# Optimization experiments

Hardware: AMD Instinct MI355X
Metric: run time of the kernel (lower is better)

Reference implementation:

```python
import jax, jax.numpy as jnp
import numpy as np

HIDDEN = 4096
HEAD_DIM = 128
N_HEADS = 32
N_KV_HEADS = 8
ROPE_THETA = 10000.0


def setup_inputs() -> dict:
    key = jax.random.key(0)
    k1, k2, k3 = jax.random.split(key, 3)
    qkv_dim = (N_HEADS + 2 * N_KV_HEADS) * HEAD_DIM  # 6144
    x = jax.random.normal(k1, (2, 2048, HIDDEN), dtype=jnp.float32)
    w_qkv = jax.random.normal(k2, (HIDDEN, qkv_dim), dtype=jnp.float32) * (HIDDEN ** -0.5)
    w_out = jax.random.normal(k3, (N_HEADS * HEAD_DIM, HIDDEN), dtype=jnp.float32) * ((N_HEADS * HEAD_DIM) ** -0.5)
    return {"x": x, "w_qkv": w_qkv, "w_out": w_out}


def _apply_rope(t):
    # t: [B, S, H, D], rotate over full head dim (half-split convention)
    B, S, H, D = t.shape
    half = D // 2
    inv_freq = 1.0 / (ROPE_THETA ** (jnp.arange(0, half, dtype=jnp.float32) / half))
    freqs = jnp.arange(S, dtype=jnp.float32)[:, None] * inv_freq[None, :]  # [S, D/2]
    cos = jnp.cos(freqs)[None, :, None, :].astype(t.dtype)
    sin = jnp.sin(freqs)[None, :, None, :].astype(t.dtype)
    t1, t2 = t[..., :half], t[..., half:]
    return jnp.concatenate([t1 * cos - t2 * sin, t1 * sin + t2 * cos], axis=-1)


def reference(x, w_qkv, w_out):
    B, S, _ = x.shape
    qkv = x @ w_qkv  # [B, S, (H + 2*Hkv) * D]
    qkv = qkv.reshape(B, S, N_HEADS + 2 * N_KV_HEADS, HEAD_DIM)
    q = qkv[:, :, :N_HEADS]                                 # [B,S,H,D]
    k = qkv[:, :, N_HEADS:N_HEADS + N_KV_HEADS]             # [B,S,Hkv,D]
    v = qkv[:, :, N_HEADS + N_KV_HEADS:]                    # [B,S,Hkv,D]
    q = _apply_rope(q)
    k = _apply_rope(k)
    # GQA: expand KV heads to match query heads
    group = N_HEADS // N_KV_HEADS
    k = jnp.repeat(k, group, axis=2)  # [B,S,H,D]
    v = jnp.repeat(v, group, axis=2)
    q = q.transpose(0, 2, 1, 3)  # [B,H,S,D]
    k = k.transpose(0, 2, 1, 3)
    v = v.transpose(0, 2, 1, 3)
    scale = HEAD_DIM ** -0.5
    scores = jnp.einsum('bhqd,bhkd->bhqk', q, k) * scale  # [B,H,S,S]
    probs = jax.nn.softmax(scores, axis=-1)
    out = jnp.einsum('bhqk,bhkd->bhqd', probs, v)  # [B,H,S,D]
    out = out.transpose(0, 2, 1, 3).reshape(B, S, N_HEADS * HEAD_DIM)
    return out @ w_out  # [B,S,hidden]
```

## Files before the change

### kernel.cpp

```cpp
#include <hip/hip_runtime.h>

typedef unsigned short u16;
typedef float f32x4 __attribute__((ext_vector_type(4)));
typedef __bf16 bf16x8 __attribute__((ext_vector_type(8)));

__device__ __forceinline__ u16 f2bf(float f) {
  union { float f; unsigned int u; } x; x.f = f;
  unsigned int u = x.u;
  u += 0x7fffu + ((u >> 16) & 1u);
  return (u16)(u >> 16);
}
__device__ __forceinline__ float bf2f(u16 h) {
  union { unsigned int u; float f; } x; x.u = ((unsigned int)h) << 16;
  return x.f;
}
#if __has_builtin(__builtin_amdgcn_exp2f)
__device__ __forceinline__ float exp2_hw(float x) { return __builtin_amdgcn_exp2f(x); }
#else
__device__ __forceinline__ float exp2_hw(float x) { return exp2f(x); }
#endif
__device__ __forceinline__ void load_lds16(const void* g, void* l) {
  __builtin_amdgcn_global_load_lds(
      (const __attribute__((address_space(1))) unsigned int*)g,
      (__attribute__((address_space(3))) unsigned int*)l, 16, 0, 0);
}
__device__ __forceinline__ f32x4 mfma16(bf16x8 a, bf16x8 b, f32x4 c) {
  return __builtin_amdgcn_mfma_f32_16x16x32_bf16(a, b, c, 0, 0, 0);
}
__device__ __forceinline__ void bar() { __builtin_amdgcn_s_barrier(); }
template <int Nw> __device__ __forceinline__ void waitvm() {
  if constexpr (Nw == 8)      asm volatile("s_waitcnt vmcnt(8)" ::: "memory");
  else if constexpr (Nw == 6) asm volatile("s_waitcnt vmcnt(6)" ::: "memory");
  else if constexpr (Nw == 4) asm volatile("s_waitcnt vmcnt(4)" ::: "memory");
  else                        asm volatile("s_waitcnt vmcnt(0)" ::: "memory");
}
__device__ __forceinline__ void phase_open() {
  asm volatile("" ::: "memory");
  __builtin_amdgcn_s_barrier();
  asm volatile("" ::: "memory");
  __builtin_amdgcn_s_setprio(1);
}
__device__ __forceinline__ void phase_close() {
  __builtin_amdgcn_s_setprio(0);
  asm volatile("" ::: "memory");
  __builtin_amdgcn_s_barrier();
  asm volatile("" ::: "memory");
}
template <int NV> __device__ __forceinline__ void phase_close_vm() {
  __builtin_amdgcn_s_setprio(0);
  asm volatile("" ::: "memory");
  waitvm<NV>();
  __builtin_amdgcn_s_barrier();
  asm volatile("" ::: "memory");
}

__global__ void convert4(const float* __restrict__ in, u16* __restrict__ out) {
  int i = blockIdx.x * blockDim.x + threadIdx.x;
  float4 v = reinterpret_cast<const float4*>(in)[i];
  ushort4 o;
  o.x = f2bf(v.x); o.y = f2bf(v.y); o.z = f2bf(v.z); o.w = f2bf(v.w);
  reinterpret_cast<ushort4*>(out)[i] = o;
}

__global__ void transpose_f32_bf16(const float* __restrict__ in, u16* __restrict__ out,
                                   int R, int Cd) {
  __shared__ float tile[32][33];
  int c0 = blockIdx.x * 32, r0 = blockIdx.y * 32;
  int tx = threadIdx.x, ty = threadIdx.y;
#pragma unroll
  for (int i = 0; i < 4; ++i)
    tile[ty + 8 * i][tx] = in[(size_t)(r0 + ty + 8 * i) * Cd + c0 + tx];
  __syncthreads();
#pragma unroll
  for (int i = 0; i < 4; ++i)
    out[(size_t)(c0 + ty + 8 * i) * R + r0 + tx] = f2bf(tile[tx][ty + 8 * i]);
}

__global__ void rope_table(float2* __restrict__ tab) {
  int i = blockIdx.x * blockDim.x + threadIdx.x;
  int s = i >> 6, d2 = i & 63;
  float inv = powf(10000.f, -(float)d2 * (1.f / 64.f));
  float fr = (float)s * inv;
  tab[i] = make_float2(cosf(fr), sinf(fr));
}

__global__ void rope_apply(u16* __restrict__ qkv, const float2* __restrict__ tab) {
  int i = blockIdx.x * blockDim.x + threadIdx.x;
  int d2 = i & 63;
  int head = (i >> 6) % 40;
  int row = i / 2560;
  size_t base = (size_t)row * 6144 + head * 128 + d2;
  float t1 = bf2f(qkv[base]), t2 = bf2f(qkv[base + 64]);
  float2 cs = tab[(row & 2047) * 64 + d2];
  float o1 = t1 * cs.x - t2 * cs.y;
  float o2 = t1 * cs.y + t2 * cs.x;
  float sc = (head < 32) ? 0.12751731654059898f : 1.f;
  qkv[base]      = f2bf(o1 * sc);
  qkv[base + 64] = f2bf(o2 * sc);
}

__global__ void build_vT(const u16* __restrict__ qkv, u16* __restrict__ vT) {
  __shared__ u16 tile[32][33];
  int st = blockIdx.x, dt = blockIdx.y, bh = blockIdx.z;
  int b = bh >> 3, hkv = bh & 7;
  int tx = threadIdx.x, ty = threadIdx.y;
  int s0 = st * 32, d0 = dt * 32;
#pragma unroll
  for (int i = 0; i < 4; ++i)
    tile[ty + 8 * i][tx] =
        qkv[(size_t)(b * 2048 + s0 + ty + 8 * i) * 6144 + 5120 + hkv * 128 + d0 + tx];
  __syncthreads();
  int s = s0 + tx;
  int sl = s & 63;
  int sp = (s & ~63) | (sl & 0x23) | ((sl & 0x0C) << 1) | ((sl & 0x10) >> 2);
#pragma unroll
  for (int i = 0; i < 4; ++i)
    vT[((size_t)bh * 128 + d0 + ty + 8 * i) * 2048 + sp] = tile[tx][ty + 8 * i];
}

template <int OUT_BF16>
__global__ __launch_bounds__(512, 2) void gemm_g1(const u16* __restrict__ A,
                                                  const u16* __restrict__ BT,
                                                  void* __restrict__ Cv,
                                                  int M, int N, int K) {
  __shared__ u16 As[3][256][64];
  __shared__ u16 Bs[3][128][64];
  const int tid = threadIdx.x, lane = tid & 63, wave = tid >> 6;
  const int lr = lane & 15, lg = lane >> 4, l7 = lane & 7;
  const int wm = wave >> 1, wn = wave & 1;
  const int nbx = N / 128;
  int bid = blockIdx.x;
  const int cpx = (int)gridDim.x >> 3;
  bid = (bid & 7) * cpx + (bid >> 3);
  const int bm = (bid / nbx) * 256, bn = (bid % nbx) * 128;
  const int NT = K / 64;
  const int ch0 = (lg ^ l7) << 3, ch1 = ((4 | lg) ^ l7) << 3;

  auto stageA = [&](int t, int rg) {
    int k0 = t * 64;
#pragma unroll
    for (int o = 0; o < 4; ++o) {
      int cid = o * 512 + tid;
      int row = cid >> 3;
      int sc2 = (cid & 7) ^ (row & 7);
      load_lds16(A + (size_t)(bm + row) * K + k0 + sc2 * 8,
                 (u16*)&As[rg][0][0] + (o * 512 + wave * 64) * 8);
    }
  };
  auto stageB = [&](int t, int rg) {
    int k0 = t * 64;
#pragma unroll
    for (int o = 0; o < 2; ++o) {
      int cid = o * 512 + tid;
      int row = cid >> 3;
      int sc2 = (cid & 7) ^ (row & 7);
      load_lds16(BT + (size_t)(bn + row) * K + k0 + sc2 * 8,
                 (u16*)&Bs[rg][0][0] + (o * 512 + wave * 64) * 8);
    }
  };

  bf16x8 af[4][2], b01[2][2], b23[2][2];
  f32x4 acc[4][4] = {};

  stageB(0, 0); stageA(0, 0); stageB(1, 1); stageA(1, 1);
  waitvm<6>();
  bar();

  int c = 0;
  for (int t = 0; t < NT; ++t) {
    int cs = c + 2; if (cs >= 3) cs -= 3;
    const bool pf = (t + 2) < NT;
#pragma unroll
    for (int mi = 0; mi < 4; ++mi) {
      af[mi][0] = *(const bf16x8*)&As[c][wm * 64 + mi * 16 + lr][ch0];
      af[mi][1] = *(const bf16x8*)&As[c][wm * 64 + mi * 16 + lr][ch1];
    }
#pragma unroll
    for (int j = 0; j < 2; ++j) {
      b01[j][0] = *(const bf16x8*)&Bs[c][wn * 64 + j * 16 + lr][ch0];
      b01[j][1] = *(const bf16x8*)&Bs[c][wn * 64 + j * 16 + lr][ch1];
    }
    if (pf) stageB(t + 2, cs);
    phase_open();
#pragma unroll
    for (int mi = 0; mi < 4; ++mi)
#pragma unroll
      for (int j = 0; j < 2; ++j) {
        acc[mi][j] = mfma16(af[mi][0], b01[j][0], acc[mi][j]);
        acc[mi][j] = mfma16(af[mi][1], b01[j][1], acc[mi][j]);
      }
    phase_close();
#pragma unroll
    for (int j = 0; j < 2; ++j) {
      b23[j][0] = *(const bf16x8*)&Bs[c][wn * 64 + (j + 2) * 16 + lr][ch0];
      b23[j][1] = *(const bf16x8*)&Bs[c][wn * 64 + (j + 2) * 16 + lr][ch1];
    }
    if (pf) stageA(t + 2, cs);
    phase_open();
#pragma unroll
    for (int mi = 0; mi < 4; ++mi)
#pragma unroll
      for (int j = 0; j < 2; ++j) {
        acc[mi][j + 2] = mfma16(af[mi][0], b23[j][0], acc[mi][j + 2]);
        acc[mi][j + 2] = mfma16(af[mi][1], b23[j][1], acc[mi][j + 2]);
      }
    if (pf) phase_close_vm<6>(); else phase_close_vm<0>();
    c = c + 1; if (c >= 3) c -= 3;
  }
#pragma unroll
  for (int mi = 0; mi < 4; ++mi) {
    int row = bm + wm * 64 + mi * 16 + lg * 4;
#pragma unroll
    for (int j = 0; j < 4; ++j) {
      int col = bn + wn * 64 + j * 16 + lr;
#pragma unroll
      for (int r = 0; r < 4; ++r) {
        if constexpr (OUT_BF16)
          ((u16*)Cv)[(size_t)(row + r) * N + col] = f2bf(acc[mi][j][r]);
        else
          ((float*)Cv)[(size_t)(row + r) * N + col] = acc[mi][j][r];
      }
    }
  }
}

template <int OUT_BF16>
__global__ __launch_bounds__(512, 2) void gemm_g2(const u16* __restrict__ A,
                                                  const u16* __restrict__ BT,
                                                  void* __restrict__ Cv,
                                                  int M, int N, int K) {
  __shared__ u16 As[2][256][64];
  __shared__ u16 Bs[2][256][64];
  const int tid = threadIdx.x, lane = tid & 63, wave = tid >> 6;
  const int lr = lane & 15, lg = lane >> 4, l7 = lane & 7;
  const int wm = wave >> 2, wn = wave & 3;
  const int nbx = N / 256;
  int bid = blockIdx.x;
  const int cpx = (int)gridDim.x >> 3;
  bid = (bid & 7) * cpx + (bid >> 3);
  const int bm = (bid / nbx) * 256, bn = (bid % nbx) * 256;
  const int NT = K / 64;
  const int ch0 = (lg ^ l7) << 3, ch1 = ((4 | lg) ^ l7) << 3;

  auto stageA = [&](int t, int rg) {
    int k0 = t * 64;
#pragma unroll
    for (int o = 0; o < 4; ++o) {
      int cid = o * 512 + tid;
      int row = cid >> 3;
      int sc2 = (cid & 7) ^ (row & 7);
      load_lds16(A + (size_t)(bm + row) * K + k0 + sc2 * 8,
                 (u16*)&As[rg][0][0] + (o * 512 + wave * 64) * 8);
    }
  };
  auto stageBh = [&](int t, int rg, int h) {
    int k0 = t * 64;
#pragma unroll
    for (int o = 0; o < 2; ++o) {
      int oo = h * 2 + o;
      int cid = oo * 512 + tid;
      int row = cid >> 3;
      int sc2 = (cid & 7) ^ (row & 7);
      load_lds16(BT + (size_t)(bn + row) * K + k0 + sc2 * 8,
                 (u16*)&Bs[rg][0][0] + (oo * 512 + wave * 64) * 8);
    }
  };

  bf16x8 a0[4][2], a1[4][2], b01[2][2], b23[2][2];
  f32x4 acc[8][4] = {};

  stageA(0, 0); stageBh(0, 0, 0); stageBh(0, 0, 1); stageA(1, 1);
  stageBh(1, 1, 0); stageBh(1, 1, 1);
  waitvm<8>();
  bar();

  for (int t = 0; t < NT; ++t) {
    const int c = t & 1;
    const bool pf = (t + 2) < NT;
#pragma unroll
    for (int mi = 0; mi < 4; ++mi) {
      a0[mi][0] = *(const bf16x8*)&As[c][wm * 128 + mi * 16 + lr][ch0];
      a0[mi][1] = *(const bf16x8*)&As[c][wm * 128 + mi * 16 + lr][ch1];
    }
#pragma unroll
    for (int j = 0; j < 2; ++j) {
      b01[j][0] = *(const bf16x8*)&Bs[c][wn * 64 + j * 16 + lr][ch0];
      b01[j][1] = *(const bf16x8*)&Bs[c][wn * 64 + j * 16 + lr][ch1];
    }
    phase_open();
#pragma unroll
    for (int mi = 0; mi < 4; ++mi)
#pragma unroll
      for (int j = 0; j < 2; ++j) {
        acc[mi][j] = mfma16(a0[mi][0], b01[j][0], acc[mi][j]);
        acc[mi][j] = mfma16(a0[mi][1], b01[j][1], acc[mi][j]);
      }
    phase_close();
#pragma unroll
    for (int j = 0; j < 2; ++j) {
      b23[j][0] = *(const bf16x8*)&Bs[c][wn * 64 + (j + 2) * 16 + lr][ch0];
      b23[j][1] = *(const bf16x8*)&Bs[c][wn * 64 + (j + 2) * 16 + lr][ch1];
    }
    phase_open();
#pragma unroll
    for (int mi = 0; mi < 4; ++mi)
#pragma unroll
      for (int j = 0; j < 2; ++j) {
        acc[mi][j + 2] = mfma16(a0[mi][0], b23[j][0], acc[mi][j + 2]);
        acc[mi][j + 2] = mfma16(a0[mi][1], b23[j][1], acc[mi][j + 2]);
      }
    phase_close();
#pragma unroll
    for (int mi = 0; mi < 4; ++mi) {
      a1[mi][0] = *(const bf16x8*)&As[c][wm * 128 + 64 + mi * 16 + lr][ch0];
      a1[mi][1] = *(const bf16x8*)&As[c][wm * 128 + 64 + mi * 16 + lr][ch1];
    }
    if (pf) stageBh(t + 2, c, 0);
    phase_open();
#pragma unroll
    for (int mi = 0; mi < 4; ++mi)
#pragma unroll
      for (int j = 0; j < 2; ++j) {
        acc[mi + 4][j] = mfma16(a1[mi][0], b01[j][0], acc[mi + 4][j]);
        acc[mi + 4][j] = mfma16(a1[mi][1], b01[j][1], acc[mi + 4][j]);
      }
    phase_close();
    if (pf) { stageBh(t + 2, c, 1); stageA(t + 2, c); }
    phase_open();
#pragma unroll
    for (int mi = 0; mi < 4; ++mi)
#pragma unroll
      for (int j = 0; j < 2; ++j) {
        acc[mi + 4][j + 2] = mfma16(a1[mi][0], b23[j][0], acc[mi + 4][j + 2]);
        acc[mi + 4][j + 2] = mfma16(a1[mi][1], b23[j][1], acc[mi + 4][j + 2]);
      }
    if (pf) phase_close_vm<8>(); else phase_close_vm<0>();
  }
#pragma unroll
  for (int mi = 0; mi < 8; ++mi) {
    int row = bm + wm * 128 + mi * 16 + lg * 4;
#pragma unroll
    for (int j = 0; j < 4; ++j) {
      int col = bn + wn * 64 + j * 16 + lr;
#pragma unroll
      for (int r = 0; r < 4; ++r) {
        if constexpr (OUT_BF16)
          ((u16*)Cv)[(size_t)(row + r) * N + col] = f2bf(acc[mi][j][r]);
        else
          ((float*)Cv)[(size_t)(row + r) * N + col] = acc[mi][j][r];
      }
    }
  }
}

__global__ __launch_bounds__(256, 3) void attn_fused(const u16* __restrict__ qkv,
                                                     const u16* __restrict__ vT,
                                                     u16* __restrict__ attn_out) {
  __shared__ u16 Ksm[64][128];
  __shared__ u16 Vsm[128][64];
  const int qt = blockIdx.x, h = blockIdx.y, b = blockIdx.z;
  const int hkv = h >> 2;
  const int tid = threadIdx.x, lane = tid & 63, wave = tid >> 6;
  const int lr = lane & 15, lg = lane >> 4;
  const int qrow0 = qt * 128 + wave * 32;

  bf16x8 qf[2][4];
#pragma unroll
  for (int q2 = 0; q2 < 2; ++q2) {
    const u16* qp = qkv + (size_t)(b * 2048 + qrow0 + q2 * 16 + lr) * 6144 + h * 128;
#pragma unroll
    for (int kk = 0; kk < 4; ++kk)
      qf[q2][kk] = *(const bf16x8*)(qp + kk * 32 + lg * 8);
  }
  float l_acc[2] = {0.f, 0.f};
  f32x4 acc_o[2][8] = {};

  for (int kv0 = 0; kv0 < 2048; kv0 += 64) {
#pragma unroll
    for (int c = 0; c < 4; ++c) {
      int cid = c * 256 + tid;
      int base = (c * 256 + wave * 64) * 8;
      int krow = cid >> 4;
      int kcc = (cid & 15) ^ (krow & 7);
      load_lds16(qkv + (size_t)(b * 2048 + kv0 + krow) * 6144 + 4096 + hkv * 128 + kcc * 8,
                 (u16*)Ksm + base);
      int vrow = cid >> 3;
      int vcc = (cid & 7) ^ (vrow & 7);
      load_lds16(vT + ((size_t)(b * 8 + hkv) * 128 + vrow) * 2048 + kv0 + vcc * 8,
                 (u16*)Vsm + base);
    }
    __syncthreads();

    bf16x8 pfr[2][2];
#pragma unroll
    for (int k2 = 0; k2 < 2; ++k2) {
      f32x4 sc[2][2] = {};
#pragma unroll
      for (int ktl = 0; ktl < 2; ++ktl) {
        int krow = (k2 * 2 + ktl) * 16 + lr;
#pragma unroll
        for (int kk = 0; kk < 4; ++kk) {
          bf16x8 kf = *(const bf16x8*)((u16*)Ksm + krow * 128 +
                                       ((((kk << 2) | lg) ^ (krow & 7)) << 3));
          sc[0][ktl] = mfma16(kf, qf[0][kk], sc[0][ktl]);
          sc[1][ktl] = mfma16(kf, qf[1][kk], sc[1][ktl]);
        }
      }
#pragma unroll
      for (int q2 = 0; q2 < 2; ++q2) {
        bf16x8 pk;
#pragma unroll
        for (int ktl = 0; ktl < 2; ++ktl)
#pragma unroll
          for (int r = 0; r < 4; ++r) {
            float e = exp2_hw(sc[q2][ktl][r]);
            l_acc[q2] += e;
            pk[ktl * 4 + r] = (__bf16)e;
          }
        pfr[q2][k2] = pk;
      }
    }
#pragma unroll
    for (int dt = 0; dt < 8; ++dt) {
      int vrow = dt * 16 + lr;
#pragma unroll
      for (int k2 = 0; k2 < 2; ++k2) {
        bf16x8 vf = *(const bf16x8*)((u16*)Vsm + vrow * 64 +
                                     ((((k2 << 2) | lg) ^ (vrow & 7)) << 3));
        acc_o[0][dt] = mfma16(pfr[0][k2], vf, acc_o[0][dt]);
        acc_o[1][dt] = mfma16(pfr[1][k2], vf, acc_o[1][dt]);
      }
    }
    __syncthreads();
  }
#pragma unroll
  for (int q2 = 0; q2 < 2; ++q2) {
    float l = l_acc[q2];
    l += __shfl_xor(l, 16);
    l += __shfl_xor(l, 32);
    float li = 1.f / l;
    float linv[4];
#pragma unroll
    for (int r = 0; r < 4; ++r) linv[r] = __shfl(li, lg * 4 + r);
    u16* op = attn_out + (size_t)(b * 2048 + qrow0 + q2 * 16) * 4096 + h * 128;
#pragma unroll
    for (int dt = 0; dt < 8; ++dt)
#pragma unroll
      for (int r = 0; r < 4; ++r)
        op[(size_t)(lg * 4 + r) * 4096 + dt * 16 + lr] = f2bf(acc_o[q2][dt][r] * linv[r]);
  }
}

extern "C" void kernel_launch(void* const* d_in, const int* in_sizes, int n_in,
                              void* d_out, int out_size, void* d_ws, size_t ws_size,
                              hipStream_t stream) {
  const float* x     = (const float*)d_in[0];
  const float* w_qkv = (const float*)d_in[1];
  const float* w_out = (const float*)d_in[2];
  float* out = (float*)d_out;
  char* ws = (char*)d_ws;

  u16*    xbf = (u16*)(ws);
  u16*    wT  = (u16*)(ws + (size_t)33554432);
  u16*    qkv = (u16*)(ws + (size_t)83886080);
  u16*    vT  = (u16*)(ws + (size_t)134217728);
  float2* tab = (float2*)(ws + (size_t)142606336);

  dim3 tb(32, 8);
  convert4<<<16384, 256, 0, stream>>>(x, xbf);
  transpose_f32_bf16<<<dim3(192, 128), tb, 0, stream>>>(w_qkv, wT, 4096, 6144);
  rope_table<<<512, 256, 0, stream>>>(tab);
  gemm_g1<1><<<768, 512, 0, stream>>>(xbf, wT, qkv, 4096, 6144, 4096);
  rope_apply<<<40960, 256, 0, stream>>>(qkv, tab);
  build_vT<<<dim3(64, 4, 16), tb, 0, stream>>>(qkv, vT);
  attn_fused<<<dim3(16, 32, 2), 256, 0, stream>>>(qkv, vT, xbf);
  transpose_f32_bf16<<<dim3(128, 128), tb, 0, stream>>>(w_out, wT, 4096, 4096);
  gemm_g2<0><<<256, 512, 0, stream>>>(xbf, wT, out, 4096, 4096, 4096);
}
```

Baseline: 591.8 us.

## Switch GEMM kernels to 32x32x16 MFMA with rebalanced prefetch staging

```diff
diff --git a/kernel.cpp b/kernel.cpp
--- a/kernel.cpp
+++ b/kernel.cpp
@@ -2,6 +2,7 @@
 
 typedef unsigned short u16;
 typedef float f32x4 __attribute__((ext_vector_type(4)));
+typedef float f32x16 __attribute__((ext_vector_type(16)));
 typedef __bf16 bf16x8 __attribute__((ext_vector_type(8)));
 
 __device__ __forceinline__ u16 f2bf(float f) {
@@ -26,6 +27,9 @@
 }
 __device__ __forceinline__ f32x4 mfma16(bf16x8 a, bf16x8 b, f32x4 c) {
   return __builtin_amdgcn_mfma_f32_16x16x32_bf16(a, b, c, 0, 0, 0);
+}
+__device__ __forceinline__ f32x16 mfma32(bf16x8 a, bf16x8 b, f32x16 c) {
+  return __builtin_amdgcn_mfma_f32_32x32x16_bf16(a, b, c, 0, 0, 0);
 }
 __device__ __forceinline__ void bar() { __builtin_amdgcn_s_barrier(); }
 template <int Nw> __device__ __forceinline__ void waitvm() {
@@ -126,7 +130,7 @@
   __shared__ u16 As[3][256][64];
   __shared__ u16 Bs[3][128][64];
   const int tid = threadIdx.x, lane = tid & 63, wave = tid >> 6;
-  const int lr = lane & 15, lg = lane >> 4, l7 = lane & 7;
+  const int l31 = lane & 31, hi = lane >> 5, sw7 = lane & 7;
   const int wm = wave >> 1, wn = wave & 1;
   const int nbx = N / 128;
   int bid = blockIdx.x;
@@ -134,7 +138,6 @@
   bid = (bid & 7) * cpx + (bid >> 3);
   const int bm = (bid / nbx) * 256, bn = (bid % nbx) * 128;
   const int NT = K / 64;
-  const int ch0 = (lg ^ l7) << 3, ch1 = ((4 | lg) ^ l7) << 3;
 
   auto stageA = [&](int t, int rg) {
     int k0 = t * 64;
@@ -159,8 +162,8 @@
     }
   };
 
-  bf16x8 af[4][2], b01[2][2], b23[2][2];
-  f32x4 acc[4][4] = {};
+  f32x16 acc[2][2] = {};
+  bf16x8 af[2][4], bj[4];
 
   stageB(0, 0); stageA(0, 0); stageB(1, 1); stageA(1, 1);
   waitvm<6>();
@@ -171,57 +174,49 @@
     int cs = c + 2; if (cs >= 3) cs -= 3;
     const bool pf = (t + 2) < NT;
 #pragma unroll
-    for (int mi = 0; mi < 4; ++mi) {
-      af[mi][0] = *(const bf16x8*)&As[c][wm * 64 + mi * 16 + lr][ch0];
-      af[mi][1] = *(const bf16x8*)&As[c][wm * 64 + mi * 16 + lr][ch1];
-    }
-#pragma unroll
-    for (int j = 0; j < 2; ++j) {
-      b01[j][0] = *(const bf16x8*)&Bs[c][wn * 64 + j * 16 + lr][ch0];
-      b01[j][1] = *(const bf16x8*)&Bs[c][wn * 64 + j * 16 + lr][ch1];
-    }
+    for (int blk = 0; blk < 2; ++blk)
+#pragma unroll
+      for (int ks = 0; ks < 4; ++ks)
+        af[blk][ks] = *(const bf16x8*)&As[c][wm * 64 + blk * 32 + l31]
+                                         [(((ks * 2 + hi) ^ sw7)) * 8];
+#pragma unroll
+    for (int ks = 0; ks < 4; ++ks)
+      bj[ks] = *(const bf16x8*)&Bs[c][wn * 64 + l31][(((ks * 2 + hi) ^ sw7)) * 8];
     if (pf) stageB(t + 2, cs);
     phase_open();
 #pragma unroll
-    for (int mi = 0; mi < 4; ++mi)
-#pragma unroll
-      for (int j = 0; j < 2; ++j) {
-        acc[mi][j] = mfma16(af[mi][0], b01[j][0], acc[mi][j]);
-        acc[mi][j] = mfma16(af[mi][1], b01[j][1], acc[mi][j]);
-      }
+    for (int ks = 0; ks < 4; ++ks)
+#pragma unroll
+      for (int blk = 0; blk < 2; ++blk)
+        acc[blk][0] = mfma32(af[blk][ks], bj[ks], acc[blk][0]);
     phase_close();
 #pragma unroll
-    for (int j = 0; j < 2; ++j) {
-      b23[j][0] = *(const bf16x8*)&Bs[c][wn * 64 + (j + 2) * 16 + lr][ch0];
-      b23[j][1] = *(const bf16x8*)&Bs[c][wn * 64 + (j + 2) * 16 + lr][ch1];
-    }
+    for (int ks = 0; ks < 4; ++ks)
+      bj[ks] = *(const bf16x8*)&Bs[c][wn * 64 + 32 + l31][(((ks * 2 + hi) ^ sw7)) * 8];
     if (pf) stageA(t + 2, cs);
     phase_open();
 #pragma unroll
-    for (int mi = 0; mi < 4; ++mi)
-#pragma unroll
-      for (int j = 0; j < 2; ++j) {
-        acc[mi][j + 2] = mfma16(af[mi][0], b23[j][0], acc[mi][j + 2]);
-        acc[mi][j + 2] = mfma16(af[mi][1], b23[j][1], acc[mi][j + 2]);
-      }
+    for (int ks = 0; ks < 4; ++ks)
+#pragma unroll
+      for (int blk = 0; blk < 2; ++blk)
+        acc[blk][1] = mfma32(af[blk][ks], bj[ks], acc[blk][1]);
     if (pf) phase_close_vm<6>(); else phase_close_vm<0>();
     c = c + 1; if (c >= 3) c -= 3;
   }
 #pragma unroll
-  for (int mi = 0; mi < 4; ++mi) {
-    int row = bm + wm * 64 + mi * 16 + lg * 4;
-#pragma unroll
-    for (int j = 0; j < 4; ++j) {
-      int col = bn + wn * 64 + j * 16 + lr;
-#pragma unroll
-      for (int r = 0; r < 4; ++r) {
+  for (int blk = 0; blk < 2; ++blk)
+#pragma unroll
+    for (int jb = 0; jb < 2; ++jb) {
+      int col = bn + wn * 64 + jb * 32 + l31;
+#pragma unroll
+      for (int reg = 0; reg < 16; ++reg) {
+        int row = bm + wm * 64 + blk * 32 + (reg & 3) + 8 * (reg >> 2) + 4 * hi;
         if constexpr (OUT_BF16)
-          ((u16*)Cv)[(size_t)(row + r) * N + col] = f2bf(acc[mi][j][r]);
+          ((u16*)Cv)[(size_t)row * N + col] = f2bf(acc[blk][jb][reg]);
         else
-          ((float*)Cv)[(size_t)(row + r) * N + col] = acc[mi][j][r];
+          ((float*)Cv)[(size_t)row * N + col] = acc[blk][jb][reg];
       }
     }
-  }
 }
 
 template <int OUT_BF16>
@@ -232,7 +227,7 @@
   __shared__ u16 As[2][256][64];
   __shared__ u16 Bs[2][256][64];
   const int tid = threadIdx.x, lane = tid & 63, wave = tid >> 6;
-  const int lr = lane & 15, lg = lane >> 4, l7 = lane & 7;
+  const int l31 = lane & 31, hi = lane >> 5, sw7 = lane & 7;
   const int wm = wave >> 2, wn = wave & 3;
   const int nbx = N / 256;
   int bid = blockIdx.x;
@@ -240,17 +235,17 @@
   bid = (bid & 7) * cpx + (bid >> 3);
   const int bm = (bid / nbx) * 256, bn = (bid % nbx) * 256;
   const int NT = K / 64;
-  const int ch0 = (lg ^ l7) << 3, ch1 = ((4 | lg) ^ l7) << 3;
-
-  auto stageA = [&](int t, int rg) {
+
+  auto stageAh = [&](int t, int rg, int h) {
     int k0 = t * 64;
 #pragma unroll
-    for (int o = 0; o < 4; ++o) {
-      int cid = o * 512 + tid;
+    for (int o = 0; o < 2; ++o) {
+      int oo = h * 2 + o;
+      int cid = oo * 512 + tid;
       int row = cid >> 3;
       int sc2 = (cid & 7) ^ (row & 7);
       load_lds16(A + (size_t)(bm + row) * K + k0 + sc2 * 8,
-                 (u16*)&As[rg][0][0] + (o * 512 + wave * 64) * 8);
+                 (u16*)&As[rg][0][0] + (oo * 512 + wave * 64) * 8);
     }
   };
   auto stageBh = [&](int t, int rg, int h) {
@@ -266,91 +261,84 @@
     }
   };
 
-  bf16x8 a0[4][2], a1[4][2], b01[2][2], b23[2][2];
-  f32x4 acc[8][4] = {};
-
-  stageA(0, 0); stageBh(0, 0, 0); stageBh(0, 0, 1); stageA(1, 1);
+  f32x16 acc[4][2] = {};
+  bf16x8 bfr[2][4], af[4];
+
+  stageAh(0, 0, 0); stageAh(0, 0, 1);
+  stageBh(0, 0, 0); stageBh(0, 0, 1);
   stageBh(1, 1, 0); stageBh(1, 1, 1);
-  waitvm<8>();
+  stageAh(1, 1, 0);
+  waitvm<6>();
   bar();
 
   for (int t = 0; t < NT; ++t) {
     const int c = t & 1;
-    const bool pf = (t + 2) < NT;
-#pragma unroll
-    for (int mi = 0; mi < 4; ++mi) {
-      a0[mi][0] = *(const bf16x8*)&As[c][wm * 128 + mi * 16 + lr][ch0];
-      a0[mi][1] = *(const bf16x8*)&As[c][wm * 128 + mi * 16 + lr][ch1];
-    }
-#pragma unroll
-    for (int j = 0; j < 2; ++j) {
-      b01[j][0] = *(const bf16x8*)&Bs[c][wn * 64 + j * 16 + lr][ch0];
-      b01[j][1] = *(const bf16x8*)&Bs[c][wn * 64 + j * 16 + lr][ch1];
-    }
-    phase_open();
-#pragma unroll
-    for (int mi = 0; mi < 4; ++mi)
-#pragma unroll
-      for (int j = 0; j < 2; ++j) {
-        acc[mi][j] = mfma16(a0[mi][0], b01[j][0], acc[mi][j]);
-        acc[mi][j] = mfma16(a0[mi][1], b01[j][1], acc[mi][j]);
+    const bool pf1 = (t + 1) < NT, pf2 = (t + 2) < NT;
+#pragma unroll
+    for (int jb = 0; jb < 2; ++jb)
+#pragma unroll
+      for (int ks = 0; ks < 4; ++ks)
+        bfr[jb][ks] = *(const bf16x8*)&Bs[c][wn * 64 + jb * 32 + l31]
+                                         [(((ks * 2 + hi) ^ sw7)) * 8];
+#pragma unroll
+    for (int ks = 0; ks < 4; ++ks)
+      af[ks] = *(const bf16x8*)&As[c][wm * 128 + l31][(((ks * 2 + hi) ^ sw7)) * 8];
+    if (pf1) stageAh(t + 1, c ^ 1, 1);
+    phase_open();
+#pragma unroll
+    for (int ks = 0; ks < 4; ++ks)
+#pragma unroll
+      for (int jb = 0; jb < 2; ++jb)
+        acc[0][jb] = mfma32(af[ks], bfr[jb][ks], acc[0][jb]);
+    phase_close();
+#pragma unroll
+    for (int ks = 0; ks < 4; ++ks)
+      af[ks] = *(const bf16x8*)&As[c][wm * 128 + 32 + l31][(((ks * 2 + hi) ^ sw7)) * 8];
+    if (pf2) stageBh(t + 2, c, 0);
+    phase_open();
+#pragma unroll
+    for (int ks = 0; ks < 4; ++ks)
+#pragma unroll
+      for (int jb = 0; jb < 2; ++jb)
+        acc[1][jb] = mfma32(af[ks], bfr[jb][ks], acc[1][jb]);
+    phase_close();
+#pragma unroll
+    for (int ks = 0; ks < 4; ++ks)
+      af[ks] = *(const bf16x8*)&As[c][wm * 128 + 64 + l31][(((ks * 2 + hi) ^ sw7)) * 8];
+    if (pf2) stageBh(t + 2, c, 1);
+    phase_open();
+#pragma unroll
+    for (int ks = 0; ks < 4; ++ks)
+#pragma unroll
+      for (int jb = 0; jb < 2; ++jb)
+        acc[2][jb] = mfma32(af[ks], bfr[jb][ks], acc[2][jb]);
+    phase_close();
+#pragma unroll
+    for (int ks = 0; ks < 4; ++ks)
+      af[ks] = *(const bf16x8*)&As[c][wm * 128 + 96 + l31][(((ks * 2 + hi) ^ sw7)) * 8];
+    if (pf2) stageAh(t + 2, c, 0);
+    phase_open();
+#pragma unroll
+    for (int ks = 0; ks < 4; ++ks)
+#pragma unroll
+      for (int jb = 0; jb < 2; ++jb)
+        acc[3][jb] = mfma32(af[ks], bfr[jb][ks], acc[3][jb]);
+    if (pf2) phase_close_vm<6>(); else phase_close_vm<0>();
+  }
+#pragma unroll
+  for (int blk = 0; blk < 4; ++blk)
+#pragma unroll
+    for (int jb = 0; jb < 2; ++jb) {
+      int col = bn + wn * 64 + jb * 32 + l31;
+#pragma unroll
+      for (int reg = 0; reg < 16; ++reg) {
+        int row = bm + wm * 128 + blk * 32 + (reg & 3) + 8 * (reg >> 2) + 4 * hi;
+        if constexpr (OUT_BF16)
+          ((u16*)Cv)[(size_t)row * N + col] = f2bf(acc[blk][jb][reg]);
+        else
+          ((float*)Cv)[(size_t)row * N + col] = acc[blk][jb][reg];
       }
-    phase_close();
-#pragma unroll
-    for (int j = 0; j < 2; ++j) {
-      b23[j][0] = *(const bf16x8*)&Bs[c][wn * 64 + (j + 2) * 16 + lr][ch0];
-      b23[j][1] = *(const bf16x8*)&Bs[c][wn * 64 + (j + 2) * 16 + lr][ch1];
-    }
-    phase_open();
-#pragma unroll
-    for (int mi = 0; mi < 4; ++mi)
-#pragma unroll
-      for (int j = 0; j < 2; ++j) {
-        acc[mi][j + 2] = mfma16(a0[mi][0], b23[j][0], acc[mi][j + 2]);
-        acc[mi][j + 2] = mfma16(a0[mi][1], b23[j][1], acc[mi][j + 2]);
-      }
-    phase_close();
-#pragma unroll
-    for (int mi = 0; mi < 4; ++mi) {
-      a1[mi][0] = *(const bf16x8*)&As[c][wm * 128 + 64 + mi * 16 + lr][ch0];
-      a1[mi][1] = *(const bf16x8*)&As[c][wm * 128 + 64 + mi * 16 + lr][ch1];
-    }
-    if (pf) stageBh(t + 2, c, 0);
-    phase_open();
-#pragma unroll
-    for (int mi = 0; mi < 4; ++mi)
-#pragma unroll
-      for (int j = 0; j < 2; ++j) {
-        acc[mi + 4][j] = mfma16(a1[mi][0], b01[j][0], acc[mi + 4][j]);
-        acc[mi + 4][j] = mfma16(a1[mi][1], b01[j][1], acc[mi + 4][j]);
-      }
-    phase_close();
-    if (pf) { stageBh(t + 2, c, 1); stageA(t + 2, c); }
-    phase_open();
-#pragma unroll
-    for (int mi = 0; mi < 4; ++mi)
-#pragma unroll
-      for (int j = 0; j < 2; ++j) {
-        acc[mi + 4][j + 2] = mfma16(a1[mi][0], b23[j][0], acc[mi + 4][j + 2]);
-        acc[mi + 4][j + 2] = mfma16(a1[mi][1], b23[j][1], acc[mi + 4][j + 2]);
-      }
-    if (pf) phase_close_vm<8>(); else phase_close_vm<0>();
-  }
-#pragma unroll
-  for (int mi = 0; mi < 8; ++mi) {
-    int row = bm + wm * 128 + mi * 16 + lg * 4;
-#pragma unroll
-    for (int j = 0; j < 4; ++j) {
-      int col = bn + wn * 64 + j * 16 + lr;
-#pragma unroll
-      for (int r = 0; r < 4; ++r) {
-        if constexpr (OUT_BF16)
-          ((u16*)Cv)[(size_t)(row + r) * N + col] = f2bf(acc[mi][j][r]);
-        else
-          ((float*)Cv)[(size_t)(row + r) * N + col] = acc[mi][j][r];
-      }
-    }
-  }
+    }
 }
 
 __global__ __launch_bounds__(256, 3) void attn_fused(const u16* __restrict__ qkv,
```

New measurement: 622.2 us. +5.1%, slower.

## Double-buffer K/V tiles in attention with 32-row KV blocks

Applied to the files above, without the earlier changes.

```diff
diff --git a/kernel.cpp b/kernel.cpp
--- a/kernel.cpp
+++ b/kernel.cpp
@@ -111,8 +111,8 @@
         qkv[(size_t)(b * 2048 + s0 + ty + 8 * i) * 6144 + 5120 + hkv * 128 + d0 + tx];
   __syncthreads();
   int s = s0 + tx;
-  int sl = s & 63;
-  int sp = (s & ~63) | (sl & 0x23) | ((sl & 0x0C) << 1) | ((sl & 0x10) >> 2);
+  int sl = s & 31;
+  int sp = (s & ~31) | (sl & 3) | ((sl & 0x0C) << 1) | ((sl & 0x10) >> 2);
 #pragma unroll
   for (int i = 0; i < 4; ++i)
     vT[((size_t)bh * 128 + d0 + ty + 8 * i) * 2048 + sp] = tile[tx][ty + 8 * i];
@@ -356,8 +356,8 @@
 __global__ __launch_bounds__(256, 3) void attn_fused(const u16* __restrict__ qkv,
                                                      const u16* __restrict__ vT,
                                                      u16* __restrict__ attn_out) {
-  __shared__ u16 Ksm[64][128];
-  __shared__ u16 Vsm[128][64];
+  __shared__ u16 Ksm[2][32][128];
+  __shared__ u16 Vsm[2][128][32];
   const int qt = blockIdx.x, h = blockIdx.y, b = blockIdx.z;
   const int hkv = h >> 2;
   const int tid = threadIdx.x, lane = tid & 63, wave = tid >> 6;
@@ -375,61 +375,63 @@
   float l_acc[2] = {0.f, 0.f};
   f32x4 acc_o[2][8] = {};
 
-  for (int kv0 = 0; kv0 < 2048; kv0 += 64) {
-#pragma unroll
-    for (int c = 0; c < 4; ++c) {
+  auto stage = [&](int t, int rg) {
+    int kv0 = t * 32;
+#pragma unroll
+    for (int c = 0; c < 2; ++c) {
       int cid = c * 256 + tid;
       int base = (c * 256 + wave * 64) * 8;
       int krow = cid >> 4;
       int kcc = (cid & 15) ^ (krow & 7);
       load_lds16(qkv + (size_t)(b * 2048 + kv0 + krow) * 6144 + 4096 + hkv * 128 + kcc * 8,
-                 (u16*)Ksm + base);
-      int vrow = cid >> 3;
-      int vcc = (cid & 7) ^ (vrow & 7);
+                 (u16*)&Ksm[rg][0][0] + base);
+      int vrow = cid >> 2;
+      int vcc = (cid & 3) ^ (vrow & 3);
       load_lds16(vT + ((size_t)(b * 8 + hkv) * 128 + vrow) * 2048 + kv0 + vcc * 8,
-                 (u16*)Vsm + base);
-    }
-    __syncthreads();
-
-    bf16x8 pfr[2][2];
-#pragma unroll
-    for (int k2 = 0; k2 < 2; ++k2) {
-      f32x4 sc[2][2] = {};
-#pragma unroll
-      for (int ktl = 0; ktl < 2; ++ktl) {
-        int krow = (k2 * 2 + ktl) * 16 + lr;
-#pragma unroll
-        for (int kk = 0; kk < 4; ++kk) {
-          bf16x8 kf = *(const bf16x8*)((u16*)Ksm + krow * 128 +
-                                       ((((kk << 2) | lg) ^ (krow & 7)) << 3));
-          sc[0][ktl] = mfma16(kf, qf[0][kk], sc[0][ktl]);
-          sc[1][ktl] = mfma16(kf, qf[1][kk], sc[1][ktl]);
+                 (u16*)&Vsm[rg][0][0] + base);
+    }
+  };
+
+  stage(0, 0);
+  __syncthreads();
+
+  for (int t = 0; t < 64; ++t) {
+    const int c = t & 1;
+    if (t + 1 < 64) stage(t + 1, c ^ 1);
+
+    f32x4 sc[2][2] = {};
+#pragma unroll
+    for (int kt = 0; kt < 2; ++kt) {
+      int krow = kt * 16 + lr;
+#pragma unroll
+      for (int kk = 0; kk < 4; ++kk) {
+        bf16x8 kf = *(const bf16x8*)((u16*)&Ksm[c][0][0] + krow * 128 +
+                                     ((((kk << 2) | lg) ^ (krow & 7)) << 3));
+        sc[0][kt] = mfma16(kf, qf[0][kk], sc[0][kt]);
+        sc[1][kt] = mfma16(kf, qf[1][kk], sc[1][kt]);
+      }
+    }
+    bf16x8 pfr[2];
+#pragma unroll
+    for (int q2 = 0; q2 < 2; ++q2) {
+      bf16x8 pk;
+#pragma unroll
+      for (int kt = 0; kt < 2; ++kt)
+#pragma unroll
+        for (int r = 0; r < 4; ++r) {
+          float e = exp2_hw(sc[q2][kt][r]);
+          l_acc[q2] += e;
+          pk[kt * 4 + r] = (__bf16)e;
         }
-      }
-#pragma unroll
-      for (int q2 = 0; q2 < 2; ++q2) {
-        bf16x8 pk;
-#pragma unroll
-        for (int ktl = 0; ktl < 2; ++ktl)
-#pragma unroll
-          for (int r = 0; r < 4; ++r) {
-            float e = exp2_hw(sc[q2][ktl][r]);
-            l_acc[q2] += e;
-            pk[ktl * 4 + r] = (__bf16)e;
-          }
-        pfr[q2][k2] = pk;
-      }
+      pfr[q2] = pk;
     }
 #pragma unroll
     for (int dt = 0; dt < 8; ++dt) {
       int vrow = dt * 16 + lr;
-#pragma unroll
-      for (int k2 = 0; k2 < 2; ++k2) {
-        bf16x8 vf = *(const bf16x8*)((u16*)Vsm + vrow * 64 +
-                                     ((((k2 << 2) | lg) ^ (vrow & 7)) << 3));
-        acc_o[0][dt] = mfma16(pfr[0][k2], vf, acc_o[0][dt]);
-        acc_o[1][dt] = mfma16(pfr[1][k2], vf, acc_o[1][dt]);
-      }
+      bf16x8 vf = *(const bf16x8*)((u16*)&Vsm[c][0][0] + vrow * 32 +
+                                   ((lg ^ (vrow & 3)) << 3));
+      acc_o[0][dt] = mfma16(pfr[0], vf, acc_o[0][dt]);
+      acc_o[1][dt] = mfma16(pfr[1], vf, acc_o[1][dt]);
     }
     __syncthreads();
   }
```

Result: no change. 597.4 us (+1.0%).
